# Kernel tuning notes

Hardware: AMD Instinct MI355X
Metric: run time of the kernel (lower is better)

## Reference

```python
import jax, jax.numpy as jnp
import numpy as np

B, S, H = 2, 2048, 3584
NH, NKV, HD = 28, 4, 128
GROUPS = NH // NKV  # 7
SCALING = HD ** -0.5
NEG = -1e9


def setup_inputs() -> dict:
    key = jax.random.key(0)
    ks = jax.random.split(key, 10)
    hidden_states = jax.random.normal(ks[0], (B, S, H), jnp.float32)
    # RoPE tables (faithful functional form; use real rotary angles)
    inv_freq = 1.0 / (1000000.0 ** (jnp.arange(0, HD, 2, dtype=jnp.float32) / HD))
    pos = jnp.arange(S, dtype=jnp.float32)
    freqs = jnp.outer(pos, inv_freq)                 # [S, HD/2]
    emb = jnp.concatenate([freqs, freqs], axis=-1)   # [S, HD]
    cos = jnp.broadcast_to(jnp.cos(emb)[None], (B, S, HD))
    sin = jnp.broadcast_to(jnp.sin(emb)[None], (B, S, HD))
    # additive causal mask [1,1,S,S]
    causal = jnp.tril(jnp.ones((S, S), dtype=bool))
    attention_mask = jnp.where(causal, 0.0, NEG).astype(jnp.float32)[None, None]
    sc = 0.02
    Wq = jax.random.normal(ks[1], (NH * HD, H), jnp.float32) * sc
    bq = jax.random.normal(ks[2], (NH * HD,), jnp.float32) * sc
    Wk = jax.random.normal(ks[3], (NKV * HD, H), jnp.float32) * sc
    bk = jax.random.normal(ks[4], (NKV * HD,), jnp.float32) * sc
    Wv = jax.random.normal(ks[5], (NKV * HD, H), jnp.float32) * sc
    bv = jax.random.normal(ks[6], (NKV * HD,), jnp.float32) * sc
    Wo = jax.random.normal(ks[7], (H, NH * HD), jnp.float32) * sc
    return dict(hidden_states=hidden_states, cos=cos, sin=sin,
                attention_mask=attention_mask, Wq=Wq, bq=bq, Wk=Wk, bk=bk,
                Wv=Wv, bv=bv, Wo=Wo)


def _rotate_half(x):
    x1, x2 = jnp.split(x, 2, axis=-1)
    return jnp.concatenate([-x2, x1], axis=-1)


def reference(hidden_states, cos, sin, attention_mask, Wq, bq, Wk, bk, Wv, bv, Wo):
    Bv_, Sv_ = hidden_states.shape[:2]
    # projections -> [B, heads, S, HD]
    q = (hidden_states @ Wq.T + bq).reshape(Bv_, Sv_, NH, HD).transpose(0, 2, 1, 3)
    k = (hidden_states @ Wk.T + bk).reshape(Bv_, Sv_, NKV, HD).transpose(0, 2, 1, 3)
    v = (hidden_states @ Wv.T + bv).reshape(Bv_, Sv_, NKV, HD).transpose(0, 2, 1, 3)
    # RoPE (unsqueeze_dim=1)
    c, s = cos[:, None], sin[:, None]
    q = q * c + _rotate_half(q) * s
    k = k * c + _rotate_half(k) * s
    # repeat_kv for GQA
    k = jnp.repeat(k, GROUPS, axis=1)  # [B, NH, S, HD]
    v = jnp.repeat(v, GROUPS, axis=1)
    scores = jnp.einsum('bhqd,bhkd->bhqk', q, k) * SCALING
    scores = scores + attention_mask[:, :, :, :k.shape[-2]]
    probs = jax.nn.softmax(scores.astype(jnp.float32), axis=-1).astype(q.dtype)
    attn = jnp.einsum('bhqk,bhkd->bhqd', probs, v)          # [B, NH, S, HD]
    attn = attn.transpose(0, 2, 1, 3).reshape(Bv_, Sv_, NH * HD)
    out = attn @ Wo.T
    return out, probs
```

## Files before the change

### kernel.cpp

```cpp
#include <hip/hip_runtime.h>

#define Bn 2
#define Sn 2048
#define Hn 3584
#define NHn 28
#define NKVn 4
#define HDn 128
#define GROUPSn 7
#define SCALEF 0.08838834764831845f
#define NOUT 14680064LL

typedef __attribute__((ext_vector_type(4))) float f4v;
typedef __attribute__((ext_vector_type(16))) float f32x16;
typedef __attribute__((ext_vector_type(8))) short bf16x8;
typedef __attribute__((ext_vector_type(4))) short s16x4;

typedef __attribute__((address_space(1))) void gvoid;
typedef __attribute__((address_space(3))) void lvoid;
#define GLL16(g, l) __builtin_amdgcn_global_load_lds((gvoid*)(void*)(g), (lvoid*)(l), 16, 0, 0)

__device__ __forceinline__ short f2bf(float f) {
  unsigned u = __builtin_bit_cast(unsigned, f);
  u = (u + 0x7fffu + ((u >> 16) & 1u)) >> 16;
  return (short)u;
}

__global__ __launch_bounds__(256) void cast_bf16(const float* __restrict__ in,
                                                 short* __restrict__ out, long long n4) {
  long long i = (long long)blockIdx.x * 256 + threadIdx.x;
  long long stride = (long long)gridDim.x * 256;
  for (; i < n4; i += stride) {
    f4v f = ((const f4v*)in)[i];
    s16x4 o = { f2bf(f.x), f2bf(f.y), f2bf(f.z), f2bf(f.w) };
    ((s16x4*)out)[i] = o;
  }
}

__global__ __launch_bounds__(256) void concat_bias(const float* __restrict__ bq,
                                                   const float* __restrict__ bk,
                                                   const float* __restrict__ bv,
                                                   float* __restrict__ out) {
  int i = blockIdx.x * 256 + threadIdx.x;
  if (i < 3584) out[i] = bq[i];
  else if (i < 4096) out[i] = bk[i - 3584];
  else if (i < 4608) out[i] = bv[i - 4096];
}

__device__ __forceinline__ void mm128_core(const short* __restrict__ Atile, long long lda,
                                           const short* __restrict__ Btile, long long ldb,
                                           int nk, short* lA, short* lB, f4v (&acc)[4][4]) {
  const int tid = threadIdx.x;
  const int lane = tid & 63;
  const int wr = (tid >> 6) >> 1, wc = (tid >> 6) & 1;
  const int srow = tid >> 2;
  const int scol = (tid & 3) * 8;
  const short* a0 = Atile + (long long)srow * lda + scol;
  const short* a1 = Atile + (long long)(srow + 64) * lda + scol;
  const short* b0 = Btile + (long long)srow * ldb + scol;
  const short* b1 = Btile + (long long)(srow + 64) * ldb + scol;
  short* la0 = lA + tid * 8;
  short* la1 = lA + (256 + tid) * 8;
  short* lb0 = lB + tid * 8;
  short* lb1 = lB + (256 + tid) * 8;
  const int fr = lane & 15;
  const int kc = (lane >> 4) * 8;
  for (int kt = 0; kt < nk; ++kt) {
    GLL16(a0 + kt * 32, la0);
    GLL16(a1 + kt * 32, la1);
    GLL16(b0 + kt * 32, lb0);
    GLL16(b1 + kt * 32, lb1);
    __syncthreads();
    bf16x8 af[4], bf[4];
#pragma unroll
    for (int m = 0; m < 4; ++m)
      af[m] = *(const bf16x8*)&lA[(wr * 64 + m * 16 + fr) * 32 + kc];
#pragma unroll
    for (int n = 0; n < 4; ++n)
      bf[n] = *(const bf16x8*)&lB[(wc * 64 + n * 16 + fr) * 32 + kc];
#pragma unroll
    for (int m = 0; m < 4; ++m)
#pragma unroll
      for (int n = 0; n < 4; ++n)
        acc[m][n] = __builtin_amdgcn_mfma_f32_16x16x32_bf16(af[m], bf[n], acc[m][n], 0, 0, 0);
    __syncthreads();
  }
}

__global__ __launch_bounds__(256) void gemm_bias_f32(const short* __restrict__ A,
                                                     const short* __restrict__ B,
                                                     float* __restrict__ C,
                                                     const float* __restrict__ bias,
                                                     int K, int N, int gx) {
  __shared__ alignas(16) short lA[4096];
  __shared__ alignas(16) short lB[4096];
  int nwg = gridDim.x * gridDim.y;
  int bid = (int)blockIdx.y * gridDim.x + (int)blockIdx.x;
  int cpx = nwg >> 3;
  int swz = (bid & 7) * cpx + (bid >> 3);
  int bx = swz % gx, by = swz / gx;
  const long long brow = (long long)by * 128;
  const long long bcol = (long long)bx * 128;
  f4v acc[4][4] = {};
  mm128_core(A + brow * K, K, B + bcol * K, K, K >> 5, lA, lB, acc);
  const int lane = threadIdx.x & 63;
  const int wr = (threadIdx.x >> 6) >> 1, wc = (threadIdx.x >> 6) & 1;
  const int rr = (lane >> 4) * 4, cc = lane & 15;
#pragma unroll
  for (int n = 0; n < 4; ++n) {
    long long col = bcol + wc * 64 + n * 16 + cc;
    float bv = bias ? bias[col] : 0.f;
#pragma unroll
    for (int m = 0; m < 4; ++m) {
#pragma unroll
      for (int j = 0; j < 4; ++j) {
        long long row = brow + wr * 64 + m * 16 + rr + j;
        C[row * N + col] = acc[m][n][j] + bv;
      }
    }
  }
}

__global__ __launch_bounds__(256) void rope_qk(const float* __restrict__ qkv,
                                               const float* __restrict__ cosb,
                                               const float* __restrict__ sinb,
                                               short* __restrict__ qo,
                                               short* __restrict__ ko) {
  long long bs = blockIdx.x;
  int b = (int)(bs >> 11);
  int s = (int)(bs & 2047);
  const float* row = qkv + bs * 4608;
  const float* cp = cosb + bs * 128;
  const float* sp = sinb + bs * 128;
  for (int i = threadIdx.x; i < 4096; i += 256) {
    int d = i & 127;
    float c = cp[d], sn = sp[d];
    float x = row[i];
    float xr = (d < 64) ? -row[i + 64] : row[i - 64];
    short v = f2bf(x * c + xr * sn);
    if (i < 3584) {
      int h = i >> 7;
      qo[(((long long)(b * NHn + h) * Sn + s)) * HDn + d] = v;
    } else {
      int h = (i - 3584) >> 7;
      ko[(((long long)(b * NKVn + h) * Sn + s)) * HDn + d] = v;
    }
  }
}

__global__ void vtrans(const float* __restrict__ qkv, short* __restrict__ vt) {
  __shared__ float tile[32][33];
  int bh = blockIdx.z;
  int b = bh >> 2, h = bh & 3;
  int s0 = blockIdx.x * 32, d0 = blockIdx.y * 32;
  int tx = threadIdx.x, ty = threadIdx.y;
#pragma unroll
  for (int j = 0; j < 32; j += 8) {
    int s = s0 + ty + j;
    tile[ty + j][tx] = qkv[((long long)(b * Sn + s)) * 4608 + 4096 + h * 128 + d0 + tx];
  }
  __syncthreads();
#pragma unroll
  for (int j = 0; j < 32; j += 8) {
    int d = d0 + ty + j;
    vt[((long long)(bh * 128 + d)) * Sn + s0 + tx] = f2bf(tile[tx][ty + j]);
  }
}

__global__ __launch_bounds__(256, 1) void fused_attn4(const short* __restrict__ Q,
                                                      const short* __restrict__ Kb,
                                                      const short* __restrict__ Vt,
                                                      float* __restrict__ probs,
                                                      short* __restrict__ attn) {
  __shared__ alignas(16) short lK[2][8192];
  __shared__ alignas(16) short lV[8192];
  const int tid = threadIdx.x;
  const int w = tid >> 6;
  const int lane = tid & 63;
  const int lam = lane & 31, h = lane >> 5;
  const int qb = 15 - (int)blockIdx.x;
  const int bh = blockIdx.y;
  const int b = bh / NHn, hh = bh - b * NHn, kv = hh / GROUPSn;
  const short* Qb = Q + (long long)bh * (Sn * HDn);
  const short* Kbb = Kb + (long long)(b * NKVn + kv) * (Sn * HDn);
  const short* Vb = Vt + (long long)(b * NKVn + kv) * (HDn * Sn);
  float* Pb = probs + (long long)bh * ((long long)Sn * Sn) + (long long)qb * 128 * Sn;
  const int qloc = w * 32 + lam;

  bf16x8 qf[8];
  {
    const short* qr = Qb + (long long)(qb * 128 + qloc) * HDn + h * 8;
#pragma unroll
    for (int s = 0; s < 8; ++s) qf[s] = *(const bf16x8*)(qr + s * 16);
  }
  int rswK[4], cswK[4];
#pragma unroll
  for (int i = 0; i < 4; ++i) {
    int M = i * 256 + tid;
    rswK[i] = M >> 4;
    cswK[i] = (M & 15) ^ (rswK[i] & 15);
  }
  int rswV[4], cswV[4];
#pragma unroll
  for (int i = 0; i < 4; ++i) {
    int M = i * 256 + tid;
    rswV[i] = M >> 3;
    cswV[i] = (M & 7) ^ (rswV[i] & 7);
  }
  const int c8 = lam & 15;
  const int v8 = lam & 7;
  const int nkt = 2 * qb + 2;

#define STAGEK(BUF, KT) do {                                                      \
    const short* base_ = Kbb + (long long)(KT) * 64 * HDn;                        \
    _Pragma("unroll")                                                             \
    for (int i = 0; i < 4; ++i)                                                   \
      GLL16(base_ + (long long)rswK[i] * HDn + cswK[i] * 8,                       \
            (short*)lK[BUF] + (i * 256 + tid) * 8);                               \
  } while (0)

#define STAGEV(KT) do {                                                           \
    _Pragma("unroll")                                                             \
    for (int i = 0; i < 4; ++i)                                                   \
      GLL16(Vb + (long long)rswV[i] * Sn + (KT) * 64 + cswV[i] * 8,               \
            lV + (i * 256 + tid) * 8);                                            \
  } while (0)

#define QKT2(ACCP, LCUR) do {                                                     \
    _Pragma("unroll")                                                             \
    for (int s = 0; s < 8; ++s) {                                                 \
      const int co_ = ((s * 2 + h) ^ c8) * 8;                                     \
      _Pragma("unroll")                                                           \
      for (int a = 0; a < 2; ++a) {                                               \
        bf16x8 kf_ = *(const bf16x8*)&(LCUR)[(a * 32 + lam) * 128 + co_];         \
        ACCP[a] = __builtin_amdgcn_mfma_f32_32x32x16_bf16(kf_, qf[s], ACCP[a], 0, 0, 0); \
      }                                                                           \
    }                                                                             \
  } while (0)

  float lsum = 0.f;
  STAGEK(0, 0);
  int cur = 0;
  for (int kt = 0; kt < nkt; ++kt) {
    __syncthreads();
    if (kt + 1 < nkt) STAGEK(cur ^ 1, kt + 1);
    const short* lcur = (const short*)lK[cur];
    f32x16 accp[2] = {};
    QKT2(accp, lcur);
    const int kbase = kt * 64 - qb * 128;
#pragma unroll
    for (int a = 0; a < 2; ++a)
#pragma unroll
      for (int r = 0; r < 16; ++r) {
        int kloc = a * 32 + (r & 3) + 8 * (r >> 2) + 4 * h;
        float s = fminf(accp[a][r] * SCALEF, 60.f);
        float p = __expf(s);
        if (kbase + kloc > qloc) p = 0.f;
        lsum += p;
      }
    cur ^= 1;
  }
  lsum += __shfl_xor(lsum, 32);
  const float invl = 1.f / lsum;

  __syncthreads();
  STAGEK(0, 0);
  cur = 0;
  f32x16 acco[4] = {};
  for (int kt = 0; kt < nkt; ++kt) {
    __syncthreads();
    if (kt + 1 < nkt) STAGEK(cur ^ 1, kt + 1);
    STAGEV(kt);
    const short* lcur = (const short*)lK[cur];
    f32x16 accp[2] = {};
    QKT2(accp, lcur);
    __syncthreads();
    const int kbase = kt * 64 - qb * 128;
    float* prow = Pb + (long long)qloc * Sn + kt * 64 + 4 * h;
#pragma unroll
    for (int a = 0; a < 2; ++a) {
      float pn[16];
#pragma unroll
      for (int r = 0; r < 16; ++r) {
        int kloc = a * 32 + (r & 3) + 8 * (r >> 2) + 4 * h;
        float s = fminf(accp[a][r] * SCALEF, 60.f);
        float p = __expf(s) * invl;
        if (kbase + kloc > qloc) p = 0.f;
        pn[r] = p;
      }
#pragma unroll
      for (int T = 0; T < 4; ++T) {
        f4v v = { pn[4 * T], pn[4 * T + 1], pn[4 * T + 2], pn[4 * T + 3] };
        *(f4v*)(prow + a * 32 + 8 * T) = v;
      }
#pragma unroll
      for (int ci = 0; ci < 2; ++ci) {
        const int ro = ci * 8;
        float r0 = __shfl_xor(h ? pn[ro + 0] : pn[ro + 4], 32);
        float r1 = __shfl_xor(h ? pn[ro + 1] : pn[ro + 5], 32);
        float r2 = __shfl_xor(h ? pn[ro + 2] : pn[ro + 6], 32);
        float r3 = __shfl_xor(h ? pn[ro + 3] : pn[ro + 7], 32);
        float t0 = h ? r0 : pn[ro + 0];
        float t1 = h ? r1 : pn[ro + 1];
        float t2 = h ? r2 : pn[ro + 2];
        float t3 = h ? r3 : pn[ro + 3];
        float t4 = h ? pn[ro + 4] : r0;
        float t5 = h ? pn[ro + 5] : r1;
        float t6 = h ? pn[ro + 6] : r2;
        float t7 = h ? pn[ro + 7] : r3;
        bf16x8 pf = { f2bf(t0), f2bf(t1), f2bf(t2), f2bf(t3),
                      f2bf(t4), f2bf(t5), f2bf(t6), f2bf(t7) };
        const int c = a * 2 + ci;
#pragma unroll
        for (int f = 0; f < 4; ++f) {
          bf16x8 vf = *(const bf16x8*)&lV[(f * 32 + lam) * 64 + ((c * 2 + h) ^ v8) * 8];
          acco[f] = __builtin_amdgcn_mfma_f32_32x32x16_bf16(pf, vf, acco[f], 0, 0, 0);
        }
      }
    }
    cur ^= 1;
  }
#undef QKT2
#undef STAGEV
#undef STAGEK

#pragma unroll
  for (int f = 0; f < 4; ++f)
#pragma unroll
    for (int r = 0; r < 16; ++r) {
      int qv = (r & 3) + 8 * (r >> 2) + 4 * h;
      long long q = (long long)qb * 128 + w * 32 + qv;
      attn[((long long)(b * Sn) + q) * Hn + hh * HDn + f * 32 + lam] = f2bf(acco[f][r]);
    }

  {
    const int r0 = tid >> 3;
    const int c0 = tid & 7;
    f4v z = {0.f, 0.f, 0.f, 0.f};
    for (int ct = qb + 1; ct < 16; ++ct) {
      float* base = Pb + (long long)ct * 128;
#pragma unroll
      for (int rr = 0; rr < 128; rr += 32) {
        f4v* rowp = (f4v*)(base + (long long)(r0 + rr) * Sn);
#pragma unroll
        for (int c = 0; c < 4; ++c) __builtin_nontemporal_store(z, &rowp[c0 + c * 8]);
      }
    }
  }
}


extern "C" void kernel_launch(void* const* d_in, const int* in_sizes, int n_in,
                              void* d_out, int out_size, void* d_ws, size_t ws_size,
                              hipStream_t stream) {
  const float* hs   = (const float*)d_in[0];
  const float* cosb = (const float*)d_in[1];
  const float* sinb = (const float*)d_in[2];
  const float* Wq = (const float*)d_in[4];
  const float* bq = (const float*)d_in[5];
  const float* Wk = (const float*)d_in[6];
  const float* bk = (const float*)d_in[7];
  const float* Wv = (const float*)d_in[8];
  const float* bv = (const float*)d_in[9];
  const float* Wo = (const float*)d_in[10];
  float* out   = (float*)d_out;
  float* probs = out + NOUT;
  char* ws = (char*)d_ws;
  short* hs_bf   = (short*)(ws + 0);
  short* attn_bf = hs_bf;
  short* wqkv_bf = (short*)(ws + 29360128LL);
  short* q_bf    = wqkv_bf;
  short* wo_bf   = (short*)(ws + 62390272LL);
  float* bias_qkv= (float*)(ws + 88080384LL);
  float* qkv     = (float*)(ws + 88098816LL);
  short* k_bf    = (short*)(ws + 163596288LL);
  short* vt_bf   = (short*)(ws + 167790592LL);

  cast_bf16<<<2048, 256, 0, stream>>>(hs, hs_bf, 3670016LL);
  cast_bf16<<<2048, 256, 0, stream>>>(Wq, wqkv_bf, 3211264LL);
  cast_bf16<<<512, 256, 0, stream>>>(Wk, wqkv_bf + 12845056LL, 458752LL);
  cast_bf16<<<512, 256, 0, stream>>>(Wv, wqkv_bf + 14680064LL, 458752LL);
  cast_bf16<<<2048, 256, 0, stream>>>(Wo, wo_bf, 3211264LL);
  concat_bias<<<18, 256, 0, stream>>>(bq, bk, bv, bias_qkv);

  gemm_bias_f32<<<dim3(36, 32), 256, 0, stream>>>(hs_bf, wqkv_bf, qkv, bias_qkv, 3584, 4608, 36);

  rope_qk<<<4096, 256, 0, stream>>>(qkv, cosb, sinb, q_bf, k_bf);
  vtrans<<<dim3(64, 4, 8), dim3(32, 8), 0, stream>>>(qkv, vt_bf);

  fused_attn4<<<dim3(16, 56), 256, 0, stream>>>(q_bf, k_bf, vt_bf, probs, attn_bf);

  gemm_bias_f32<<<dim3(28, 32), 256, 0, stream>>>(attn_bf, wo_bf, out, nullptr, 3584, 3584, 28);
}
```

Measured before the change: 892.9 us.

## Use persistent GEMM with K=64 swizzled LDS tiles and reorder attention K staging

The GEMM core now stages 64-wide K slices per iteration with an XOR-swizzled LDS layout, which halves the number of barriers per K and avoids LDS bank conflicts. Both projection GEMMs become persistent kernels that loop over grouped tiles on a fixed grid of 768 blocks. In the attention kernel, the prefetch of the next K tile moves after the second barrier, so it no longer contends with the QK^T reads of the current tile. LDS use per GEMM block doubles, which may lower occupancy, and the persistent grid can leave a tail imbalance.

```diff
diff --git a/kernel.cpp b/kernel.cpp
--- a/kernel.cpp
+++ b/kernel.cpp
@@ -46,75 +46,80 @@
   else if (i < 4608) out[i] = bv[i - 4096];
 }
 
-__device__ __forceinline__ void mm128_core(const short* __restrict__ Atile, long long lda,
-                                           const short* __restrict__ Btile, long long ldb,
-                                           int nk, short* lA, short* lB, f4v (&acc)[4][4]) {
+__device__ __forceinline__ void mm128x64_core(const short* __restrict__ Atile, long long lda,
+                                              const short* __restrict__ Btile, long long ldb,
+                                              int nk, short* lA, short* lB, f4v (&acc)[4][4]) {
   const int tid = threadIdx.x;
   const int lane = tid & 63;
   const int wr = (tid >> 6) >> 1, wc = (tid >> 6) & 1;
-  const int srow = tid >> 2;
-  const int scol = (tid & 3) * 8;
-  const short* a0 = Atile + (long long)srow * lda + scol;
-  const short* a1 = Atile + (long long)(srow + 64) * lda + scol;
-  const short* b0 = Btile + (long long)srow * ldb + scol;
-  const short* b1 = Btile + (long long)(srow + 64) * ldb + scol;
-  short* la0 = lA + tid * 8;
-  short* la1 = lA + (256 + tid) * 8;
-  short* lb0 = lB + tid * 8;
-  short* lb1 = lB + (256 + tid) * 8;
   const int fr = lane & 15;
-  const int kc = (lane >> 4) * 8;
+  const int g = lane >> 4;
+  int rsw[4], csw[4];
+#pragma unroll
+  for (int i = 0; i < 4; ++i) {
+    int M = i * 256 + tid;
+    rsw[i] = M >> 3;
+    csw[i] = (M & 7) ^ (rsw[i] & 7);
+  }
   for (int kt = 0; kt < nk; ++kt) {
-    GLL16(a0 + kt * 32, la0);
-    GLL16(a1 + kt * 32, la1);
-    GLL16(b0 + kt * 32, lb0);
-    GLL16(b1 + kt * 32, lb1);
-    __syncthreads();
-    bf16x8 af[4], bf[4];
-#pragma unroll
-    for (int m = 0; m < 4; ++m)
-      af[m] = *(const bf16x8*)&lA[(wr * 64 + m * 16 + fr) * 32 + kc];
-#pragma unroll
-    for (int n = 0; n < 4; ++n)
-      bf[n] = *(const bf16x8*)&lB[(wc * 64 + n * 16 + fr) * 32 + kc];
-#pragma unroll
-    for (int m = 0; m < 4; ++m)
-#pragma unroll
-      for (int n = 0; n < 4; ++n)
-        acc[m][n] = __builtin_amdgcn_mfma_f32_16x16x32_bf16(af[m], bf[n], acc[m][n], 0, 0, 0);
-    __syncthreads();
-  }
-}
-
-__global__ __launch_bounds__(256) void gemm_bias_f32(const short* __restrict__ A,
-                                                     const short* __restrict__ B,
-                                                     float* __restrict__ C,
-                                                     const float* __restrict__ bias,
-                                                     int K, int N, int gx) {
-  __shared__ alignas(16) short lA[4096];
-  __shared__ alignas(16) short lB[4096];
-  int nwg = gridDim.x * gridDim.y;
-  int bid = (int)blockIdx.y * gridDim.x + (int)blockIdx.x;
-  int cpx = nwg >> 3;
-  int swz = (bid & 7) * cpx + (bid >> 3);
-  int bx = swz % gx, by = swz / gx;
-  const long long brow = (long long)by * 128;
-  const long long bcol = (long long)bx * 128;
-  f4v acc[4][4] = {};
-  mm128_core(A + brow * K, K, B + bcol * K, K, K >> 5, lA, lB, acc);
+#pragma unroll
+    for (int i = 0; i < 4; ++i) {
+      GLL16(Atile + (long long)rsw[i] * lda + kt * 64 + csw[i] * 8, lA + (i * 256 + tid) * 8);
+      GLL16(Btile + (long long)rsw[i] * ldb + kt * 64 + csw[i] * 8, lB + (i * 256 + tid) * 8);
+    }
+    __syncthreads();
+#pragma unroll
+    for (int kk = 0; kk < 2; ++kk) {
+      bf16x8 af[4], bf[4];
+#pragma unroll
+      for (int m = 0; m < 4; ++m) {
+        int r = wr * 64 + m * 16 + fr;
+        af[m] = *(const bf16x8*)&lA[r * 64 + ((kk * 4 + g) ^ (r & 7)) * 8];
+      }
+#pragma unroll
+      for (int n = 0; n < 4; ++n) {
+        int r = wc * 64 + n * 16 + fr;
+        bf[n] = *(const bf16x8*)&lB[r * 64 + ((kk * 4 + g) ^ (r & 7)) * 8];
+      }
+#pragma unroll
+      for (int m = 0; m < 4; ++m)
+#pragma unroll
+        for (int n = 0; n < 4; ++n)
+          acc[m][n] = __builtin_amdgcn_mfma_f32_16x16x32_bf16(af[m], bf[n], acc[m][n], 0, 0, 0);
+    }
+    __syncthreads();
+  }
+}
+
+__global__ __launch_bounds__(256) void gemm_persist(const short* __restrict__ A,
+                                                    const short* __restrict__ B,
+                                                    float* __restrict__ C,
+                                                    const float* __restrict__ bias,
+                                                    int K, int N, int gx, int ntiles) {
+  __shared__ alignas(16) short lA[8192];
+  __shared__ alignas(16) short lB[8192];
+  const int nt8 = ntiles >> 3;
   const int lane = threadIdx.x & 63;
   const int wr = (threadIdx.x >> 6) >> 1, wc = (threadIdx.x >> 6) & 1;
   const int rr = (lane >> 4) * 4, cc = lane & 15;
-#pragma unroll
-  for (int n = 0; n < 4; ++n) {
-    long long col = bcol + wc * 64 + n * 16 + cc;
-    float bv = bias ? bias[col] : 0.f;
-#pragma unroll
-    for (int m = 0; m < 4; ++m) {
-#pragma unroll
-      for (int j = 0; j < 4; ++j) {
-        long long row = brow + wr * 64 + m * 16 + rr + j;
-        C[row * N + col] = acc[m][n][j] + bv;
+  for (int vt = blockIdx.x; vt < ntiles; vt += gridDim.x) {
+    const int tile = (vt & 7) * nt8 + (vt >> 3);
+    const int bx = tile % gx, by = tile / gx;
+    const long long brow = (long long)by * 128;
+    const long long bcol = (long long)bx * 128;
+    f4v acc[4][4] = {};
+    mm128x64_core(A + brow * K, K, B + bcol * K, K, K >> 6, lA, lB, acc);
+#pragma unroll
+    for (int n = 0; n < 4; ++n) {
+      long long col = bcol + wc * 64 + n * 16 + cc;
+      float bv = bias ? bias[col] : 0.f;
+#pragma unroll
+      for (int m = 0; m < 4; ++m) {
+#pragma unroll
+        for (int j = 0; j < 4; ++j) {
+          long long row = brow + wr * 64 + m * 16 + rr + j;
+          C[row * N + col] = acc[m][n][j] + bv;
+        }
       }
     }
   }
@@ -166,7 +171,7 @@
   }
 }
 
-__global__ __launch_bounds__(256, 1) void fused_attn4(const short* __restrict__ Q,
+__global__ __launch_bounds__(256, 1) void fused_attn6(const short* __restrict__ Q,
                                                       const short* __restrict__ Kb,
                                                       const short* __restrict__ Vt,
                                                       float* __restrict__ probs,
@@ -268,12 +273,12 @@
   f32x16 acco[4] = {};
   for (int kt = 0; kt < nkt; ++kt) {
     __syncthreads();
-    if (kt + 1 < nkt) STAGEK(cur ^ 1, kt + 1);
     STAGEV(kt);
     const short* lcur = (const short*)lK[cur];
     f32x16 accp[2] = {};
     QKT2(accp, lcur);
     __syncthreads();
+    if (kt + 1 < nkt) STAGEK(cur ^ 1, kt + 1);
     const int kbase = kt * 64 - qb * 128;
     float* prow = Pb + (long long)qloc * Sn + kt * 64 + 4 * h;
 #pragma unroll
@@ -382,12 +387,12 @@
   cast_bf16<<<2048, 256, 0, stream>>>(Wo, wo_bf, 3211264LL);
   concat_bias<<<18, 256, 0, stream>>>(bq, bk, bv, bias_qkv);
 
-  gemm_bias_f32<<<dim3(36, 32), 256, 0, stream>>>(hs_bf, wqkv_bf, qkv, bias_qkv, 3584, 4608, 36);
+  gemm_persist<<<768, 256, 0, stream>>>(hs_bf, wqkv_bf, qkv, bias_qkv, 3584, 4608, 36, 1152);
 
   rope_qk<<<4096, 256, 0, stream>>>(qkv, cosb, sinb, q_bf, k_bf);
   vtrans<<<dim3(64, 4, 8), dim3(32, 8), 0, stream>>>(qkv, vt_bf);
 
-  fused_attn4<<<dim3(16, 56), 256, 0, stream>>>(q_bf, k_bf, vt_bf, probs, attn_bf);
-
-  gemm_bias_f32<<<dim3(28, 32), 256, 0, stream>>>(attn_bf, wo_bf, out, nullptr, 3584, 3584, 28);
-}
+  fused_attn6<<<dim3(16, 56), 256, 0, stream>>>(q_bf, k_bf, vt_bf, probs, attn_bf);
+
+  gemm_persist<<<768, 256, 0, stream>>>(attn_bf, wo_bf, out, nullptr, 3584, 3584, 28, 896);
+}
```

New measurement: 870.3 us. 1.03x faster.
